# Kernel tuning notes

Measured on AMD Instinct MI355X. Metric: run time of the kernel, lower is better.

Reference implementation:

```python
import jax, jax.numpy as jnp
import numpy as np

B, C, H, W, K = 64, 64, 32, 32, 512  # batch, embedding_dim, latent HxW, num_embeddings
COMMITMENT_COST = 0.25


def setup_inputs() -> dict:
    key = jax.random.key(0)
    k1, k2 = jax.random.split(key)
    inputs = jax.random.normal(k1, (B, C, H, W), dtype=jnp.float32)
    # nn.Embedding weight initialized uniform(-1/K, 1/K)
    weight = jax.random.uniform(k2, (K, C), minval=-1.0 / K, maxval=1.0 / K, dtype=jnp.float32)
    return {"inputs": inputs, "weight": weight}


def reference(inputs, weight):
    # NCHW -> NHWC
    x = jnp.transpose(inputs, (0, 2, 3, 1))  # [B,H,W,C]
    b, h, w, c = x.shape
    flat = x.reshape(-1, c)  # [N, C], N = B*H*W

    distances = (jnp.sum(flat * flat, axis=1, keepdims=True)
                 + jnp.sum(weight * weight, axis=1)[None, :]
                 - 2.0 * flat @ weight.T)

    idx = jnp.argmin(distances, axis=1)  # [N]
    encodings = jax.nn.one_hot(idx, weight.shape[0], dtype=flat.dtype)  # [N, K]

    # gather codebook vectors (same math as encodings @ weight)
    quantized = weight[idx].reshape(x.shape)  # [B,H,W,C]

    e_latent = jnp.mean((jax.lax.stop_gradient(quantized) - x) ** 2, axis=(1, 2, 3))
    q_latent = jnp.mean((quantized - jax.lax.stop_gradient(x)) ** 2, axis=(1, 2, 3))
    loss = q_latent + COMMITMENT_COST * e_latent  # [B]

    # straight-through estimator
    quantized_st = x + jax.lax.stop_gradient(quantized - x)

    avg_probs = jnp.mean(encodings, axis=0)  # [K]
    perplexity = jnp.exp(-jnp.sum(avg_probs * jnp.log(avg_probs + 1e-10)))

    q_out = jnp.transpose(quantized_st, (0, 3, 1, 2))  # back to NCHW
    enc_idx = idx.reshape(b, -1)  # [B, H*W]
    return (q_out, loss, perplexity, encodings, enc_idx, distances)
```

## Files before the change

kernel.cpp:

```cpp
#include <hip/hip_runtime.h>
#include <stdint.h>
#include <math.h>

#pragma clang fp contract(off)

#define B_   64
#define C_   64
#define HW_  1024
#define K_   512
#define N_   65536

#define OUT_Q    0ull
#define OUT_LOSS 4194304ull
#define OUT_PERP 4194368ull
#define OUT_ENC  4194369ull
#define OUT_IDX  37748801ull
#define OUT_DIST 37814337ull

#define WS_WT     0ull
#define WS_WNORM  131072ull
#define WS_HIST   133120ull
#define WS_SUMSQ  135168ull
#define WS_ZERO_BYTES (512*4 + 64*4)

__global__ __launch_bounds__(256) void vq_prep(const float* __restrict__ w,
                                               float* __restrict__ wt,
                                               float* __restrict__ wnorm) {
  const int t = threadIdx.x;
  const int g = blockIdx.x * 256 + t;
  const int c = g >> 9;
  const int k = g & 511;
  wt[g] = w[k * 64 + c];

  if (blockIdx.x < 16) {
    const int row = g >> 3;
    const int j = g & 7;
    float s = 0.f;
    for (int i = 0; i < 8; ++i) {
      float v = w[row * 64 + 8 * i + j];
      float sq = v * v;
      s = s + sq;
    }
    float o1 = __shfl_xor(s, 1); s = s + o1;
    float o2 = __shfl_xor(s, 2); s = s + o2;
    float o4 = __shfl_xor(s, 4); s = s + o4;
    if (j == 0) wnorm[row] = s;
  }
}

__global__ __launch_bounds__(256, 3) void vq_main(const float* __restrict__ x,
                                                  const float* __restrict__ wt,
                                                  const float* __restrict__ wnorm,
                                                  float* __restrict__ out,
                                                  int* __restrict__ hist,
                                                  float* __restrict__ sumsq) {
  __shared__ float x_s[64 * 32];
  __shared__ float w_s[16 * 512];
  __shared__ float wn_s[512];
  __shared__ float an_s[32];
  __shared__ int   kmin_s[32];
  __shared__ float red_s[4];

  const int t   = threadIdx.x;
  const int blk = blockIdx.x;
  const int n0  = blk * 32;
  const int b   = n0 >> 10;
  const int hw0 = n0 & 1023;
  const int wid = t >> 6;
  const int l   = t & 63;

  {
    const float* xb = x + (size_t)b * 65536 + hw0;
    const int c0 = t >> 3;
    const int m4 = (t & 7) * 4;
    for (int i = 0; i < 2; ++i) {
      int c = i * 32 + c0;
      float4 v = *(const float4*)(xb + (size_t)c * 1024 + m4);
      *(float4*)(&x_s[c * 32 + m4]) = v;
    }
  }
  wn_s[t] = wnorm[t];
  wn_s[t + 256] = wnorm[t + 256];
  __syncthreads();

  {
    const int r = t >> 3, j = t & 7;
    float s = 0.f;
    for (int i = 0; i < 8; ++i) {
      float v = x_s[(8 * i + j) * 32 + r];
      float sq = v * v;
      s = s + sq;
    }
    float o1 = __shfl_xor(s, 1); s = s + o1;
    float o2 = __shfl_xor(s, 2); s = s + o2;
    float o4 = __shfl_xor(s, 4); s = s + o4;
    if (j == 0) an_s[r] = s;
  }

  float wn[8];
  for (int j = 0; j < 8; ++j) wn[j] = wn_s[l + 64 * j];

  float acc[8][8];
  for (int i = 0; i < 8; ++i)
    for (int j = 0; j < 8; ++j) acc[i][j] = 0.f;

#pragma unroll 1
  for (int cc = 0; cc < 4; ++cc) {
    __syncthreads();
    for (int i = 0; i < 8; ++i) {
      int f4 = i * 256 + t;
      *(float4*)(&w_s[f4 * 4]) = *(const float4*)(wt + (size_t)cc * 8192 + f4 * 4);
    }
    __syncthreads();
#pragma unroll
    for (int cl = 0; cl < 16; ++cl) {
      const int c = cc * 16 + cl;
      float xv[8];
      *(float4*)(xv)     = *(const float4*)(&x_s[c * 32 + 8 * wid]);
      *(float4*)(xv + 4) = *(const float4*)(&x_s[c * 32 + 8 * wid + 4]);
      float wv[8];
      for (int j = 0; j < 8; ++j) wv[j] = w_s[cl * 512 + l + 64 * j];
      for (int i = 0; i < 8; ++i)
        for (int j = 0; j < 8; ++j)
          acc[i][j] = __builtin_fmaf(xv[i], wv[j], acc[i][j]);
    }
  }

  float* const dist_o = out + OUT_DIST;
  float* const enc_o  = out + OUT_ENC;
  const int m_base = 8 * wid;
  for (int i = 0; i < 8; ++i) {
    const int m = m_base + i;
    const size_t n = (size_t)(n0 + m);
    const float an = an_s[m];
    float D[8];
    for (int j = 0; j < 8; ++j) {
      float tt = an + wn[j];
      D[j] = __builtin_fmaf(-2.f, acc[i][j], tt);
    }
    float vb = D[0]; int kb = l;
    for (int j = 1; j < 8; ++j) {
      if (D[j] < vb) { vb = D[j]; kb = l + 64 * j; }
    }
    for (int d = 1; d < 64; d <<= 1) {
      float v2 = __shfl_xor(vb, d);
      int   k2 = __shfl_xor(kb, d);
      if (v2 < vb || (v2 == vb && k2 < kb)) { vb = v2; kb = k2; }
    }
    const size_t rb = n * 512 + l;
    for (int j = 0; j < 8; ++j) dist_o[rb + 64 * j] = D[j];
    for (int j = 0; j < 8; ++j) enc_o[rb + 64 * j] = (l + 64 * j == kb) ? 1.f : 0.f;
    if (l == i) {
      out[OUT_IDX + n] = (float)kb;
      atomicAdd(&hist[kb], 1);
      kmin_s[m] = kb;
    }
  }
  __syncthreads();

  float lsum = 0.f;
  float* const q_o = out + OUT_Q;
  for (int it = 0; it < 8; ++it) {
    const int idx8 = it * 256 + t;
    const int c = idx8 >> 5, m = idx8 & 31;
    const int kb = kmin_s[m];
    const float qv = wt[(size_t)c * 512 + kb];
    const float xv = x_s[c * 32 + m];
    const float d = qv - xv;
    lsum = __builtin_fmaf(d, d, lsum);
    q_o[(size_t)b * 65536 + (size_t)c * 1024 + (hw0 + m)] = qv;
  }
  for (int d = 1; d < 64; d <<= 1) lsum += __shfl_xor(lsum, d);
  if (l == 0) red_s[wid] = lsum;
  __syncthreads();
  if (t == 0) {
    float s = (red_s[0] + red_s[1]) + (red_s[2] + red_s[3]);
    atomicAdd(sumsq + b, s);
  }
}

__global__ __launch_bounds__(512) void vq_fin(const int* __restrict__ hist,
                                              const float* __restrict__ sumsq,
                                              float* __restrict__ out) {
  __shared__ double red[8];
  const int t = threadIdx.x;
  double p = (double)hist[t] * (1.0 / 65536.0);
  double term = p * log(p + 1e-10);
  for (int d = 1; d < 64; d <<= 1) term += __shfl_xor(term, d);
  if ((t & 63) == 0) red[t >> 6] = term;
  __syncthreads();
  if (t == 0) {
    double s = 0.0;
    for (int i = 0; i < 8; ++i) s += red[i];
    out[OUT_PERP] = (float)exp(-s);
  }
  if (t < 64) {
    float m = sumsq[t] * (1.0f / 65536.0f);
    out[OUT_LOSS + t] = m + 0.25f * m;
  }
}

extern "C" void kernel_launch(void* const* d_in, const int* in_sizes, int n_in,
                              void* d_out, int out_size, void* d_ws, size_t ws_size,
                              hipStream_t stream) {
  const float* x = (const float*)d_in[0];
  const float* w = (const float*)d_in[1];
  float* out = (float*)d_out;
  char* ws = (char*)d_ws;
  float* wt    = (float*)(ws + WS_WT);
  float* wnorm = (float*)(ws + WS_WNORM);
  int*   hist  = (int*)  (ws + WS_HIST);
  float* sumsq = (float*)(ws + WS_SUMSQ);

  (void)hipMemsetAsync(ws + WS_HIST, 0, WS_ZERO_BYTES, stream);
  vq_prep<<<128, 256, 0, stream>>>(w, wt, wnorm);
  vq_main<<<2048, 256, 0, stream>>>(x, wt, wnorm, out, hist, sumsq);
  vq_fin<<<1, 512, 0, stream>>>(hist, sumsq, out);
}
```

Measured before the change: 360.5 us.

## Stream codebook from global in registers and use nontemporal vector stores

Removes the shared-memory staging of the transposed codebook and its barriers. Each lane now loads float4 codebook slices straight from global (L2-resident) with one-step register prefetch, and the k-mapping changes to 4*l+j. The large distance, one-hot and quantized outputs are written as 128-bit nontemporal stores instead of strided scalar stores, which reduces store instructions and cache pollution. The argmin shuffles are batched across the 8 rows for more ILP, and occupancy is raised to 4 blocks per CU. The risks are extra global/L2 load traffic and register pressure under the tighter launch bound.

```diff
diff --git a/kernel.cpp b/kernel.cpp
--- a/kernel.cpp
+++ b/kernel.cpp
@@ -22,6 +22,14 @@
 #define WS_HIST   133120ull
 #define WS_SUMSQ  135168ull
 #define WS_ZERO_BYTES (512*4 + 64*4)
+
+typedef float f32x4 __attribute__((ext_vector_type(4)));
+
+static __device__ __forceinline__ void nt_store4(float* p, float a, float b,
+                                                 float c, float d) {
+  f32x4 v = {a, b, c, d};
+  __builtin_nontemporal_store(v, (f32x4*)p);
+}
 
 __global__ __launch_bounds__(256) void vq_prep(const float* __restrict__ w,
                                                float* __restrict__ wt,
@@ -48,15 +56,13 @@
   }
 }
 
-__global__ __launch_bounds__(256, 3) void vq_main(const float* __restrict__ x,
+__global__ __launch_bounds__(256, 4) void vq_main(const float* __restrict__ x,
                                                   const float* __restrict__ wt,
                                                   const float* __restrict__ wnorm,
                                                   float* __restrict__ out,
                                                   int* __restrict__ hist,
                                                   float* __restrict__ sumsq) {
   __shared__ float x_s[64 * 32];
-  __shared__ float w_s[16 * 512];
-  __shared__ float wn_s[512];
   __shared__ float an_s[32];
   __shared__ int   kmin_s[32];
   __shared__ float red_s[4];
@@ -73,19 +79,19 @@
     const float* xb = x + (size_t)b * 65536 + hw0;
     const int c0 = t >> 3;
     const int m4 = (t & 7) * 4;
+#pragma unroll
     for (int i = 0; i < 2; ++i) {
       int c = i * 32 + c0;
       float4 v = *(const float4*)(xb + (size_t)c * 1024 + m4);
       *(float4*)(&x_s[c * 32 + m4]) = v;
     }
   }
-  wn_s[t] = wnorm[t];
-  wn_s[t + 256] = wnorm[t + 256];
   __syncthreads();
 
   {
     const int r = t >> 3, j = t & 7;
     float s = 0.f;
+#pragma unroll
     for (int i = 0; i < 8; ++i) {
       float v = x_s[(8 * i + j) * 32 + r];
       float sq = v * v;
@@ -98,78 +104,115 @@
   }
 
   float wn[8];
-  for (int j = 0; j < 8; ++j) wn[j] = wn_s[l + 64 * j];
+  *(float4*)(wn)     = *(const float4*)(wnorm + 4 * l);
+  *(float4*)(wn + 4) = *(const float4*)(wnorm + 256 + 4 * l);
 
   float acc[8][8];
+#pragma unroll
   for (int i = 0; i < 8; ++i)
+#pragma unroll
     for (int j = 0; j < 8; ++j) acc[i][j] = 0.f;
 
-#pragma unroll 1
-  for (int cc = 0; cc < 4; ++cc) {
-    __syncthreads();
-    for (int i = 0; i < 8; ++i) {
-      int f4 = i * 256 + t;
-      *(float4*)(&w_s[f4 * 4]) = *(const float4*)(wt + (size_t)cc * 8192 + f4 * 4);
-    }
-    __syncthreads();
-#pragma unroll
-    for (int cl = 0; cl < 16; ++cl) {
-      const int c = cc * 16 + cl;
-      float xv[8];
-      *(float4*)(xv)     = *(const float4*)(&x_s[c * 32 + 8 * wid]);
-      *(float4*)(xv + 4) = *(const float4*)(&x_s[c * 32 + 8 * wid + 4]);
-      float wv[8];
-      for (int j = 0; j < 8; ++j) wv[j] = w_s[cl * 512 + l + 64 * j];
-      for (int i = 0; i < 8; ++i)
-        for (int j = 0; j < 8; ++j)
-          acc[i][j] = __builtin_fmaf(xv[i], wv[j], acc[i][j]);
+  const float* const wl = wt + 4 * l;
+  const float* const xw = x_s + 8 * wid;
+  float4 w0 = *(const float4*)(wl);
+  float4 w1 = *(const float4*)(wl + 256);
+#pragma unroll 2
+  for (int c = 0; c < 64; ++c) {
+    const int cn = (c + 1) & 63;
+    const float4 nw0 = *(const float4*)(wl + cn * 512);
+    const float4 nw1 = *(const float4*)(wl + cn * 512 + 256);
+    float xv[8];
+    *(float4*)(xv)     = *(const float4*)(xw + c * 32);
+    *(float4*)(xv + 4) = *(const float4*)(xw + c * 32 + 4);
+    const float wv0[4] = {w0.x, w0.y, w0.z, w0.w};
+    const float wv1[4] = {w1.x, w1.y, w1.z, w1.w};
+#pragma unroll
+    for (int i = 0; i < 8; ++i) {
+#pragma unroll
+      for (int j = 0; j < 4; ++j) {
+        acc[i][j]     = __builtin_fmaf(xv[i], wv0[j], acc[i][j]);
+        acc[i][j + 4] = __builtin_fmaf(xv[i], wv1[j], acc[i][j + 4]);
+      }
+    }
+    w0 = nw0; w1 = nw1;
+  }
+
+  const int m_base = 8 * wid;
+  float vb[8]; int kb[8];
+#pragma unroll
+  for (int i = 0; i < 8; ++i) {
+    const float an = an_s[m_base + i];
+#pragma unroll
+    for (int j = 0; j < 8; ++j) {
+      float tt = an + wn[j];
+      acc[i][j] = __builtin_fmaf(-2.f, acc[i][j], tt);
+    }
+    float v = acc[i][0]; int k = 4 * l;
+#pragma unroll
+    for (int j = 1; j < 8; ++j) {
+      const int kj = ((j >> 2) << 8) + 4 * l + (j & 3);
+      if (acc[i][j] < v) { v = acc[i][j]; k = kj; }
+    }
+    vb[i] = v; kb[i] = k;
+  }
+
+#pragma unroll
+  for (int d = 1; d < 64; d <<= 1) {
+#pragma unroll
+    for (int i = 0; i < 8; ++i) {
+      float v2 = __shfl_xor(vb[i], d);
+      int   k2 = __shfl_xor(kb[i], d);
+      if (v2 < vb[i] || (v2 == vb[i] && k2 < kb[i])) { vb[i] = v2; kb[i] = k2; }
     }
   }
 
   float* const dist_o = out + OUT_DIST;
   float* const enc_o  = out + OUT_ENC;
-  const int m_base = 8 * wid;
+#pragma unroll
   for (int i = 0; i < 8; ++i) {
     const int m = m_base + i;
     const size_t n = (size_t)(n0 + m);
-    const float an = an_s[m];
-    float D[8];
-    for (int j = 0; j < 8; ++j) {
-      float tt = an + wn[j];
-      D[j] = __builtin_fmaf(-2.f, acc[i][j], tt);
-    }
-    float vb = D[0]; int kb = l;
-    for (int j = 1; j < 8; ++j) {
-      if (D[j] < vb) { vb = D[j]; kb = l + 64 * j; }
-    }
-    for (int d = 1; d < 64; d <<= 1) {
-      float v2 = __shfl_xor(vb, d);
-      int   k2 = __shfl_xor(kb, d);
-      if (v2 < vb || (v2 == vb && k2 < kb)) { vb = v2; kb = k2; }
-    }
-    const size_t rb = n * 512 + l;
-    for (int j = 0; j < 8; ++j) dist_o[rb + 64 * j] = D[j];
-    for (int j = 0; j < 8; ++j) enc_o[rb + 64 * j] = (l + 64 * j == kb) ? 1.f : 0.f;
+    float* dr = dist_o + n * 512;
+    float* er = enc_o  + n * 512;
+    nt_store4(dr + 4 * l,       acc[i][0], acc[i][1], acc[i][2], acc[i][3]);
+    nt_store4(dr + 256 + 4 * l, acc[i][4], acc[i][5], acc[i][6], acc[i][7]);
+    const int kbi = kb[i];
+    const int k0 = 4 * l;
+    nt_store4(er + 4 * l,
+              (k0 + 0 == kbi) ? 1.f : 0.f, (k0 + 1 == kbi) ? 1.f : 0.f,
+              (k0 + 2 == kbi) ? 1.f : 0.f, (k0 + 3 == kbi) ? 1.f : 0.f);
+    nt_store4(er + 256 + 4 * l,
+              (k0 + 256 == kbi) ? 1.f : 0.f, (k0 + 257 == kbi) ? 1.f : 0.f,
+              (k0 + 258 == kbi) ? 1.f : 0.f, (k0 + 259 == kbi) ? 1.f : 0.f);
     if (l == i) {
-      out[OUT_IDX + n] = (float)kb;
-      atomicAdd(&hist[kb], 1);
-      kmin_s[m] = kb;
+      out[OUT_IDX + n] = (float)kbi;
+      atomicAdd(&hist[kbi], 1);
+      kmin_s[m] = kbi;
     }
   }
   __syncthreads();
 
   float lsum = 0.f;
   float* const q_o = out + OUT_Q;
-  for (int it = 0; it < 8; ++it) {
-    const int idx8 = it * 256 + t;
-    const int c = idx8 >> 5, m = idx8 & 31;
-    const int kb = kmin_s[m];
-    const float qv = wt[(size_t)c * 512 + kb];
-    const float xv = x_s[c * 32 + m];
-    const float d = qv - xv;
-    lsum = __builtin_fmaf(d, d, lsum);
-    q_o[(size_t)b * 65536 + (size_t)c * 1024 + (hw0 + m)] = qv;
-  }
+#pragma unroll
+  for (int it = 0; it < 2; ++it) {
+    const int c  = it * 32 + (t >> 3);
+    const int m4 = (t & 7) * 4;
+    float xq[4];
+    *(float4*)(xq) = *(const float4*)(&x_s[c * 32 + m4]);
+    float qv[4];
+#pragma unroll
+    for (int u = 0; u < 4; ++u) {
+      const int kbm = kmin_s[m4 + u];
+      qv[u] = wt[(size_t)c * 512 + kbm];
+      const float d = qv[u] - xq[u];
+      lsum = __builtin_fmaf(d, d, lsum);
+    }
+    nt_store4(&q_o[(size_t)b * 65536 + (size_t)c * 1024 + hw0 + m4],
+              qv[0], qv[1], qv[2], qv[3]);
+  }
+#pragma unroll
   for (int d = 1; d < 64; d <<= 1) lsum += __shfl_xor(lsum, d);
   if (l == 0) red_s[wid] = lsum;
   __syncthreads();
```

Result: no change. 354.6 us (-1.6%).
